# Kernel optimization log

Hardware: AMD Instinct MI355X
Metric: run time of the kernel (lower is better)

Reference implementation:

```python
import jax, jax.numpy as jnp
import numpy as np

D = 2048      # d_model
H = 16        # n_heads
DH = 128      # head dim
ROPE = 64     # qk_rope_dim = dh//2
NOPE = 64     # qk_nope_dim = dh//2
QP = 1024     # q_proj_dim = int(D*0.5)
KVP = 1365    # kv_proj_dim = int(D*2/3)
THETA = 10000.0
B, S = 2, 2048


def _ln(x, w, b):
    m = x.mean(-1, keepdims=True)
    v = ((x - m) ** 2).mean(-1, keepdims=True)
    return (x - m) / jnp.sqrt(v + 1e-5) * w + b


def _rot_half(x):
    x1, x2 = jnp.split(x, 2, axis=-1)
    return jnp.concatenate([-x2, x1], axis=-1)


def _rope_tables(seq_len):
    # freqs over full dh (as in torch buffer), then slice first ROPE//2 and repeat(...,2)
    freqs = 1.0 / (THETA ** (jnp.arange(0, DH, 2, dtype=jnp.float32) / DH))  # (DH//2,)
    emb = jnp.arange(seq_len, dtype=jnp.float32)[:, None] * freqs[None, :]   # (S, DH//2)
    c = jnp.cos(emb)[:, : ROPE // 2]
    s = jnp.sin(emb)[:, : ROPE // 2]
    cos = jnp.concatenate([c, c], axis=-1)  # (S, ROPE)  matches .repeat(1,1,1,2)
    sin = jnp.concatenate([s, s], axis=-1)
    return cos, sin


def setup_inputs() -> dict:
    ks = jax.random.split(jax.random.key(0), 8)
    p = lambda i, shape: 0.01 * jax.random.normal(ks[i], shape, dtype=jnp.float32)
    return {
        "query": jax.random.normal(ks[0], (B, S, D), dtype=jnp.float32),
        "W_dq": p(1, (D, QP)),
        "W_uq": p(2, (QP, D)),
        "q_ln_w": jnp.ones((QP,), jnp.float32),
        "q_ln_b": jnp.zeros((QP,), jnp.float32),
        "W_dkv": p(3, (D, KVP + ROPE)),
        "W_ukv": p(4, (KVP, D + H * NOPE)),
        "kv_ln_w": jnp.ones((KVP,), jnp.float32),
        "kv_ln_b": jnp.zeros((KVP,), jnp.float32),
        "W_o": p(5, (D, D)),
    }


def reference(query, W_dq, W_uq, q_ln_w, q_ln_b, W_dkv, W_ukv, kv_ln_w, kv_ln_b, W_o):
    b, sq, _ = query.shape
    # Q low-rank path
    cq = _ln(query @ W_dq, q_ln_w, q_ln_b)                       # (B,S,QP)
    Q = (cq @ W_uq).reshape(b, sq, H, DH).transpose(0, 2, 1, 3)  # (B,H,S,DH)
    Qn, Qr = Q[..., :NOPE], Q[..., NOPE:]
    cos, sin = _rope_tables(sq)                                  # (S,ROPE)
    Qr = Qr * cos + _rot_half(Qr) * sin
    # KV low-rank path
    compressed_kv = query @ W_dkv                                # (B,S,KVP+ROPE)
    kv_lat, Kr = compressed_kv[..., :KVP], compressed_kv[..., KVP:]
    kv_lat = _ln(kv_lat, kv_ln_w, kv_ln_b)
    KV = (kv_lat @ W_ukv).reshape(b, sq, H, DH + NOPE).transpose(0, 2, 1, 3)
    Kn, V = KV[..., :NOPE], KV[..., NOPE:]                       # (B,H,S,NOPE),(B,H,S,DH)
    Kr = Kr * cos + _rot_half(Kr) * sin                          # (B,S,ROPE) shared head
    qh = jnp.concatenate([Qn, Qr], axis=-1)                      # (B,H,S,DH)
    kh = jnp.concatenate([Kn, jnp.broadcast_to(Kr[:, None], (b, H, sq, ROPE))], axis=-1)
    # causal attention, scale 1/sqrt(dh) as in SDPA
    scores = jnp.einsum('bhqd,bhkd->bhqk', qh, kh) / jnp.sqrt(jnp.float32(DH))
    mask = jnp.tril(jnp.ones((sq, sq), dtype=bool))
    scores = jnp.where(mask, scores, -jnp.inf)
    attn = jax.nn.softmax(scores, axis=-1)
    out = jnp.einsum('bhqk,bhkd->bhqd', attn, V).transpose(0, 2, 1, 3).reshape(b, sq, D)
    output = out @ W_o.T                                          # nn.Linear, no bias
    return output, compressed_kv
```

## Files before the change

kernel.cpp:

```cpp
#include <hip/hip_runtime.h>

#define BB_   2
#define S_    2048
#define D_    2048
#define H_    16
#define DH_   128
#define ROPE_ 64
#define QP_   1024
#define KVP_  1365
#define KVPR_ 1429
#define KVP_PAD_ 1408
#define NKV_PAD_ 1536
#define NCOMB_ 2560
#define MT_   4096
#define UKV_N_ 3072

typedef unsigned short u16;
typedef unsigned int   u32;
typedef __attribute__((ext_vector_type(4))) u16    u16x4;
typedef __attribute__((ext_vector_type(8))) u16    u16x8;
typedef __attribute__((ext_vector_type(4))) u32    u32x4;
typedef __attribute__((ext_vector_type(8))) __bf16 bf16x8;
typedef __attribute__((ext_vector_type(4))) float  f32x4;
typedef __attribute__((ext_vector_type(16))) float f32x16;

#define NEG_BIG (-1.0e30f)
#define F32_FLAG_BITS 0x49742400u

__device__ __forceinline__ float bf2f(u16 u) {
    u32 x = ((u32)u) << 16;
    return __builtin_bit_cast(float, x);
}
__device__ __forceinline__ u16 f2bf(float f) {
    u32 u = __builtin_bit_cast(u32, f);
    u32 r = u + 0x7fffu + ((u >> 16) & 1u);
    return (u16)(r >> 16);
}
__device__ __forceinline__ u32 pk2(float a, float b) {
    __bf16 x = (__bf16)a, y = (__bf16)b;
    return (u32)__builtin_bit_cast(u16, x) | ((u32)__builtin_bit_cast(u16, y) << 16);
}
__device__ __forceinline__ bf16x8 ld_bf8(const u16* p) {
    u16x8 v = *(const u16x8*)p;
    return __builtin_bit_cast(bf16x8, v);
}
__device__ __forceinline__ bool flag_f32(const u32* flag) { return flag[0] > F32_FLAG_BITS; }

__device__ __forceinline__ void async16(const void* g, void* l) {
    __builtin_amdgcn_global_load_lds(
        (const __attribute__((address_space(1))) void*)g,
        (__attribute__((address_space(3))) void*)l, 16, 0, 0);
}

__global__ __launch_bounds__(256) void detect_kernel(const u16* __restrict__ q, u32* __restrict__ flag)
{
    u32 m = 0;
    for (int i = blockIdx.x * 256 + threadIdx.x; i < (1 << 20); i += 64 * 256) {
        float v = fabsf(bf2f(q[i]));
        u32 b = __builtin_bit_cast(u32, v);
        m = m > b ? m : b;
    }
    #pragma unroll
    for (int off = 32; off; off >>= 1) {
        u32 o = (u32)__shfl_xor((int)m, off, 64);
        m = m > o ? m : o;
    }
    if ((threadIdx.x & 63) == 0) atomicMax(flag, m);
}

__global__ __launch_bounds__(256) void cast_bf16_kernel(
    const void* __restrict__ in, u16* __restrict__ out, long n, const u32* __restrict__ flag)
{
    bool f32 = flag_f32(flag);
    long i0 = ((long)blockIdx.x * 256 + threadIdx.x) * 8;
    if (i0 >= n) return;
    u16x8 o;
    if (f32) {
        const float* p = (const float*)in + i0;
        #pragma unroll
        for (int j = 0; j < 8; j++) o[j] = f2bf(p[j]);
    } else {
        o = *(const u16x8*)((const u16*)in + i0);
    }
    *(u16x8*)(out + i0) = o;
}

template <int MODE>
__global__ __launch_bounds__(256) void gemm_bt(
    const u16* __restrict__ A, const u16* __restrict__ Bt,
    void* __restrict__ Cout, int M, int N, int K, const u32* __restrict__ flag)
{
    __shared__ u16 As[2][128 * 32];
    __shared__ u16 Bs[2][128 * 32];
    const int tid  = threadIdx.x;
    const int lane = tid & 63;
    const int wave = tid >> 6;
    const int m0 = blockIdx.x * 128;
    const int n0 = blockIdx.y * 128;
    const int wr = (wave >> 1) * 64;
    const int wc = (wave & 1) * 64;
    const bool f32o = (MODE == 2) ? flag_f32(flag) : false;

    const int srow = lane >> 2;
    const int scol = (lane & 3) * 8;
    const u16* aptr0 = A  + (long)(m0 + wave * 32 + srow) * K + scol;
    const u16* bptr0 = Bt + (long)(n0 + wave * 32 + srow) * K + scol;
    const int woff = (wave * 32) * 32;

    f32x4 acc[4][4] = {};

    const int row16 = lane & 15;
    const int kq = (lane >> 4) * 8;

    auto stage = [&](int buf, int kt) {
        u16* asl = &As[buf][woff];
        u16* bsl = &Bs[buf][woff];
        async16(aptr0 + kt,          asl);
        async16(aptr0 + 16 * K + kt, asl + 16 * 32);
        async16(bptr0 + kt,          bsl);
        async16(bptr0 + 16 * K + kt, bsl + 16 * 32);
    };
    auto compute = [&](int buf) {
        bf16x8 a[4], b[4];
        #pragma unroll
        for (int i = 0; i < 4; i++)
            a[i] = ld_bf8(&As[buf][(wr + i * 16 + row16) * 32 + kq]);
        #pragma unroll
        for (int j = 0; j < 4; j++)
            b[j] = ld_bf8(&Bs[buf][(wc + j * 16 + row16) * 32 + kq]);
        #pragma unroll
        for (int i = 0; i < 4; i++)
            #pragma unroll
            for (int j = 0; j < 4; j++)
                acc[i][j] = __builtin_amdgcn_mfma_f32_16x16x32_bf16(a[i], b[j], acc[i][j], 0, 0, 0);
    };

    stage(0, 0);
    __syncthreads();
    const int nk = K >> 5;
    for (int t = 0; t < nk; t += 2) {
        stage(1, (t + 1) * 32);
        compute(0);
        __syncthreads();
        if (t + 2 < nk) stage(0, (t + 2) * 32);
        compute(1);
        __syncthreads();
    }

    const int crow = wr + (lane >> 4) * 4;
    const int ccol = wc + row16;
    #pragma unroll
    for (int i = 0; i < 4; i++) {
        #pragma unroll
        for (int r = 0; r < 4; r++) {
            long row = m0 + crow + i * 16 + r;
            #pragma unroll
            for (int j = 0; j < 4; j++) {
                float v = acc[i][j][r];
                long col = n0 + ccol + j * 16;
                if (MODE == 2 && f32o) ((float*)Cout)[row * N + col] = v;
                else                   ((u16*)Cout)[row * N + col] = f2bf(v);
            }
        }
    }
}

__global__ __launch_bounds__(256) void transpose_pad_kernel(
    const void* __restrict__ in, u16* __restrict__ out,
    int Rin, int Cin, int Nout, int Kpad, const u32* __restrict__ flag)
{
    __shared__ u16 t[32][33];
    bool f32 = flag_f32(flag);
    int k0 = blockIdx.x * 32, n0 = blockIdx.y * 32;
    int tx = threadIdx.x & 31, ty = threadIdx.x >> 5;
    #pragma unroll
    for (int rr = 0; rr < 4; ++rr) {
        int k = k0 + ty + rr * 8, n = n0 + tx;
        u16 v = 0;
        if (k < Rin && n < Cin)
            v = f32 ? f2bf(((const float*)in)[(long)k * Cin + n])
                    : ((const u16*)in)[(long)k * Cin + n];
        t[ty + rr * 8][tx] = v;
    }
    __syncthreads();
    #pragma unroll
    for (int rr = 0; rr < 4; ++rr) {
        int n = n0 + ty + rr * 8, k = k0 + tx;
        if (n < Nout && k < Kpad) out[(long)n * Kpad + k] = t[tx][ty + rr * 8];
    }
}

__device__ __forceinline__ float block_sum(float v, float* red) {
    #pragma unroll
    for (int off = 32; off; off >>= 1) v += __shfl_xor(v, off, 64);
    int wv = threadIdx.x >> 6;
    __syncthreads();
    if ((threadIdx.x & 63) == 0) red[wv] = v;
    __syncthreads();
    return red[0] + red[1] + red[2] + red[3];
}

__global__ __launch_bounds__(256) void ln_q_kernel(
    const u16* __restrict__ x, const void* __restrict__ w, const void* __restrict__ bb,
    u16* __restrict__ y, const u32* __restrict__ flag, int stride)
{
    __shared__ float red[4];
    bool f32 = flag_f32(flag);
    long row = blockIdx.x;
    const u16* xr = x + row * stride;
    float v[4]; float s = 0.f;
    #pragma unroll
    for (int i = 0; i < 4; i++) { v[i] = bf2f(xr[threadIdx.x + i * 256]); s += v[i]; }
    float mean = block_sum(s, red) * (1.0f / QP_);
    float var = 0.f;
    #pragma unroll
    for (int i = 0; i < 4; i++) { float d = v[i] - mean; var += d * d; }
    var = block_sum(var, red) * (1.0f / QP_);
    float rstd = rsqrtf(var + 1e-5f);
    #pragma unroll
    for (int i = 0; i < 4; i++) {
        int idx = threadIdx.x + i * 256;
        float wv = f32 ? ((const float*)w)[idx] : bf2f(((const u16*)w)[idx]);
        float bv = f32 ? ((const float*)bb)[idx] : bf2f(((const u16*)bb)[idx]);
        y[row * QP_ + idx] = f2bf((v[i] - mean) * rstd * wv + bv);
    }
}

__global__ __launch_bounds__(256) void ln_kv_kernel(
    const u16* __restrict__ x, const void* __restrict__ w, const void* __restrict__ bb,
    u16* __restrict__ kv_lat, void* __restrict__ d_out, const u32* __restrict__ flag, int stride)
{
    __shared__ float red[4];
    bool f32 = flag_f32(flag);
    long row = blockIdx.x;
    const u16* xr = x + row * stride;
    u16 u[6]; float v[6]; float s = 0.f;
    #pragma unroll
    for (int i = 0; i < 6; i++) {
        int idx = threadIdx.x + i * 256;
        u[i] = xr[idx];
        v[i] = bf2f(u[i]);
        if (idx < KVP_) s += v[i];
    }
    float mean = block_sum(s, red) * (1.0f / KVP_);
    float var = 0.f;
    #pragma unroll
    for (int i = 0; i < 6; i++) {
        int idx = threadIdx.x + i * 256;
        if (idx < KVP_) { float d = v[i] - mean; var += d * d; }
    }
    var = block_sum(var, red) * (1.0f / KVP_);
    float rstd = rsqrtf(var + 1e-5f);

    float* out1f = (float*)d_out + (size_t)MT_ * D_;
    u16*   out1h = (u16*)d_out   + (size_t)MT_ * D_;
    #pragma unroll
    for (int i = 0; i < 6; i++) {
        int idx = threadIdx.x + i * 256;
        if (idx < KVPR_) {
            if (f32) out1f[row * KVPR_ + idx] = v[i];
            else     out1h[row * KVPR_ + idx] = u[i];
        }
        if (idx < KVP_PAD_) {
            float wv = 0.f, bv = 0.f;
            if (idx < KVP_) {
                wv = f32 ? ((const float*)w)[idx] : bf2f(((const u16*)w)[idx]);
                bv = f32 ? ((const float*)bb)[idx] : bf2f(((const u16*)bb)[idx]);
            }
            u16 o = 0;
            if (idx < KVP_) o = f2bf((v[i] - mean) * rstd * wv + bv);
            kv_lat[row * KVP_PAD_ + idx] = o;
        }
    }
}

__global__ void rope_tab_kernel(float* __restrict__ cosT, float* __restrict__ sinT, u32* __restrict__ flag) {
    int idx = blockIdx.x * 256 + threadIdx.x;
    if (idx == 0) flag[0] = 0u;
    if (idx >= S_ * 32) return;
    int pos = idx >> 5, i = idx & 31;
    float freq = (float)exp(-((double)i / 64.0) * log(10000.0));
    float ang = (float)pos * freq;
    cosT[idx] = (float)cos((double)ang);
    sinT[idx] = (float)sin((double)ang);
}

__global__ __launch_bounds__(256) void pack_q_kernel(
    const u16* __restrict__ Qm, const float* __restrict__ cosT, const float* __restrict__ sinT,
    u16* __restrict__ qh)
{
    int bs = blockIdx.x; int b = bs >> 11; int s = bs & 2047;
    int h = threadIdx.x >> 4; int d0 = (threadIdx.x & 15) * 8;
    const u16* src = Qm + (long)bs * 2048 + h * 128 + d0;
    u16x8 val = *(const u16x8*)src;
    if (d0 >= 64) {
        int r0 = d0 - 64;
        const u16* rb = Qm + (long)bs * 2048 + h * 128 + 64;
        u16x8 out;
        #pragma unroll
        for (int j = 0; j < 8; j++) {
            int r = r0 + j; int m = r & 31;
            float c = cosT[s * 32 + m], sn = sinT[s * 32 + m];
            float x = bf2f(val[j]);
            float o = (r < 32) ? -bf2f(rb[r + 32]) : bf2f(rb[r - 32]);
            out[j] = f2bf(x * c + o * sn);
        }
        val = out;
    }
    *(u16x8*)&qh[(((long)(b * H_ + h)) * S_ + s) * 128 + d0] = val;
}

__global__ __launch_bounds__(256) void pack_kh_kernel(
    const u16* __restrict__ KV, const void* __restrict__ d_out,
    const float* __restrict__ cosT, const float* __restrict__ sinT,
    u16* __restrict__ kh, const u32* __restrict__ flag)
{
    bool f32 = flag_f32(flag);
    int bs = blockIdx.x; int b = bs >> 11; int s = bs & 2047;
    int h = threadIdx.x >> 4; int d0 = (threadIdx.x & 15) * 8;
    u16x8 val;
    if (d0 < 64) {
        val = *(const u16x8*)&KV[(long)bs * 3072 + h * 192 + d0];
    } else {
        int r0 = d0 - 64;
        const float* rf = (const float*)d_out + (size_t)MT_ * D_ + (long)bs * KVPR_ + KVP_;
        const u16*   rh = (const u16*)d_out   + (size_t)MT_ * D_ + (long)bs * KVPR_ + KVP_;
        #pragma unroll
        for (int j = 0; j < 8; j++) {
            int r = r0 + j; int m = r & 31;
            float xr = f32 ? rf[r] : bf2f(rh[r]);
            float xo = f32 ? ((r < 32) ? -rf[r + 32] : rf[r - 32])
                           : ((r < 32) ? -bf2f(rh[r + 32]) : bf2f(rh[r - 32]));
            val[j] = f2bf(xr * cosT[s * 32 + m] + xo * sinT[s * 32 + m]);
        }
    }
    *(u16x8*)&kh[(((long)(b * H_ + h)) * S_ + s) * 128 + d0] = val;
}

__global__ __launch_bounds__(256) void pack_vt_kernel(const u16* __restrict__ KV, u16* __restrict__ Vt)
{
    int bh = blockIdx.x; int b = bh >> 4, h = bh & 15;
    int s0 = blockIdx.y * 64;
    __shared__ u16 t[64][136];
    #pragma unroll
    for (int it = 0; it < 4; ++it) {
        int ch = threadIdx.x + it * 256;
        int sr = ch >> 4, c8 = (ch & 15) * 8;
        *(u16x8*)&t[sr][c8] = *(const u16x8*)&KV[((long)(b * S_ + s0 + sr)) * 3072 + h * 192 + 64 + c8];
    }
    __syncthreads();
    #pragma unroll
    for (int it = 0; it < 4; ++it) {
        int ch = threadIdx.x + it * 256;
        int d = ch >> 3, s8 = (ch & 7) * 8;
        u16x8 v;
        #pragma unroll
        for (int j = 0; j < 8; j++) v[j] = t[s8 + j][d];
        *(u16x8*)&Vt[((long)bh * 128 + d) * S_ + s0 + s8] = v;
    }
}

#define ATT_SCALE 0.08838834764831845f
#define K_LOG2E (ATT_SCALE * 1.4426950408889634f)
#define DEFER_THR 62.0f

__global__ __launch_bounds__(256, 2) void attn_kernel(
    const u16* __restrict__ qh, const u16* __restrict__ kh,
    const u16* __restrict__ Vt, u16* __restrict__ attn_out)
{
    __shared__ u16 Ks[64 * 128];
    __shared__ u16 Vs[128 * 64];

    const int bh = (int)blockIdx.x + ((int)blockIdx.z << 3);
    const int b = bh >> 4, h = bh & 15;
    const int jq = ((int)blockIdx.z < 2) ? (15 - (int)blockIdx.y) : (int)blockIdx.y;
    const int qbase = jq * 128;
    const int tid = threadIdx.x;
    const int lane = tid & 63;
    const int w = tid >> 6;
    const int l5 = lane & 31;
    const int hi = lane >> 5;
    const int wq0 = qbase + w * 32;
    const int qg = wq0 + l5;
    const int kend = qbase + 128;
    const int kend_w = wq0 + 32;

    bf16x8 qb[8];
    {
        const u16* qp = &qh[((long)bh * S_ + qg) * 128 + 8 * hi];
        #pragma unroll
        for (int kc = 0; kc < 8; kc++)
            qb[kc] = ld_bf8(qp + kc * 16);
    }

    f32x16 o[4] = {};
    float m_run = NEG_BIG;
    float l_run = 0.f;

    const long khb = (long)bh * S_;

    u16x8 kst[4], vst[4];
    auto load_kv = [&](int k0) {
        #pragma unroll
        for (int it = 0; it < 4; ++it) {
            int r = w * 16 + it * 4 + (lane >> 4);
            kst[it] = *(const u16x8*)&kh[(khb + k0 + r) * 128 + (((lane & 15) ^ (r & 7)) << 3)];
        }
        #pragma unroll
        for (int it = 0; it < 4; ++it) {
            int d = w * 32 + it * 8 + (lane >> 3);
            vst[it] = *(const u16x8*)&Vt[((long)bh * 128 + d) * S_ + k0 + (((lane & 7) ^ (d & 7)) << 3)];
        }
    };

    load_kv(0);

    for (int k0 = 0; k0 < kend; k0 += 64) {
        __syncthreads();
        #pragma unroll
        for (int it = 0; it < 4; ++it)
            *(u16x8*)&Ks[(w * 16 + it * 4) * 128 + lane * 8] = kst[it];
        #pragma unroll
        for (int it = 0; it < 4; ++it)
            *(u16x8*)&Vs[(w * 32 + it * 8) * 64 + lane * 8] = vst[it];
        __syncthreads();
        if (k0 + 64 < kend) load_kv(k0 + 64);

        if (k0 < kend_w) {
            f32x16 sc[2] = {};
            #pragma unroll
            for (int kc = 0; kc < 8; kc++) {
                #pragma unroll
                for (int ct = 0; ct < 2; ct++) {
                    int krow = ct * 32 + l5;
                    bf16x8 kf = ld_bf8(&Ks[krow * 128 + (((2 * kc + hi) ^ (krow & 7)) << 3)]);
                    sc[ct] = __builtin_amdgcn_mfma_f32_32x32x16_bf16(kf, qb[kc], sc[ct], 0, 0, 0);
                }
            }
            if (k0 + 64 > wq0) {
                #pragma unroll
                for (int ct = 0; ct < 2; ct++)
                    #pragma unroll
                    for (int g = 0; g < 4; g++)
                        #pragma unroll
                        for (int t = 0; t < 4; t++)
                            sc[ct][g * 4 + t] =
                                (k0 + ct * 32 + g * 8 + t + 4 * hi <= qg) ? sc[ct][g * 4 + t] : NEG_BIG;
            }
            float m = sc[0][0];
            #pragma unroll
            for (int i = 1; i < 16; i++) m = fmaxf(m, sc[0][i]);
            #pragma unroll
            for (int i = 0; i < 16; i++) m = fmaxf(m, sc[1][i]);
            m = fmaxf(m, __shfl_xor(m, 32, 64));
            bool ok = (m <= m_run + DEFER_THR);
            if (!__all((int)ok)) {
                float mn = fmaxf(m_run, m);
                float alpha = exp2f((m_run - mn) * K_LOG2E);
                m_run = mn;
                l_run *= alpha;
                #pragma unroll
                for (int dt = 0; dt < 4; dt++)
                    #pragma unroll
                    for (int i = 0; i < 16; i++) o[dt][i] *= alpha;
            }
            float mk = m_run * K_LOG2E;
            float s = 0.f;
            #pragma unroll
            for (int ct = 0; ct < 2; ct++)
                #pragma unroll
                for (int i = 0; i < 16; i++) {
                    float p = exp2f(fmaf(sc[ct][i], K_LOG2E, -mk));
                    sc[ct][i] = p;
                    s += p;
                }
            l_run += s + __shfl_xor(s, 32, 64);
            bf16x8 pb[4];
            #pragma unroll
            for (int ct = 0; ct < 2; ct++)
                #pragma unroll
                for (int c2 = 0; c2 < 2; c2++) {
                    u32 lo0 = pk2(sc[ct][8 * c2 + 0], sc[ct][8 * c2 + 1]);
                    u32 lo1 = pk2(sc[ct][8 * c2 + 2], sc[ct][8 * c2 + 3]);
                    u32 h0  = pk2(sc[ct][8 * c2 + 4], sc[ct][8 * c2 + 5]);
                    u32 h1  = pk2(sc[ct][8 * c2 + 6], sc[ct][8 * c2 + 7]);
                    u32 s0 = hi ? lo0 : h0;
                    u32 s1 = hi ? lo1 : h1;
                    u32 r0 = (u32)__shfl_xor((int)s0, 32, 64);
                    u32 r1 = (u32)__shfl_xor((int)s1, 32, 64);
                    u32x4 f;
                    f[0] = hi ? r0 : lo0;
                    f[1] = hi ? r1 : lo1;
                    f[2] = hi ? h0 : r0;
                    f[3] = hi ? h1 : r1;
                    pb[ct * 2 + c2] = __builtin_bit_cast(bf16x8, f);
                }
            #pragma unroll
            for (int kk = 0; kk < 4; kk++) {
                #pragma unroll
                for (int dt = 0; dt < 4; dt++) {
                    int drow = dt * 32 + l5;
                    bf16x8 vf = ld_bf8(&Vs[drow * 64 + (((2 * kk + hi) ^ (drow & 7)) << 3)]);
                    o[dt] = __builtin_amdgcn_mfma_f32_32x32x16_bf16(vf, pb[kk], o[dt], 0, 0, 0);
                }
            }
        }
    }

    float inv = 1.0f / l_run;
    const long orow = ((long)b * S_ + qg) * 2048 + h * 128;
    #pragma unroll
    for (int dt = 0; dt < 4; dt++)
        #pragma unroll
        for (int g = 0; g < 4; g++) {
            u16x4 v;
            #pragma unroll
            for (int t = 0; t < 4; t++) v[t] = f2bf(o[dt][g * 4 + t] * inv);
            *(u16x4*)&attn_out[orow + dt * 32 + g * 8 + 4 * hi] = v;
        }
}

#define MIB(x) ((size_t)(x) << 20)
extern "C" void kernel_launch(void* const* d_in, const int* in_sizes, int n_in,
                              void* d_out, int out_size, void* d_ws, size_t ws_size,
                              hipStream_t stream)
{
    const void* query  = d_in[0];
    const void* W_dq   = d_in[1];
    const void* W_uq   = d_in[2];
    const void* q_ln_w = d_in[3];
    const void* q_ln_b = d_in[4];
    const void* W_dkv  = d_in[5];
    const void* W_ukv  = d_in[6];
    const void* kv_ln_w = d_in[7];
    const void* kv_ln_b = d_in[8];
    const void* W_o    = d_in[9];
    (void)ws_size; (void)in_sizes; (void)n_in; (void)out_size;

    char* base = (char*)d_ws;
    u32*   flag     = (u32*)base;
    float* rope_cos = (float*)(base + 4096);
    float* rope_sin = (float*)(base + 266240);
    u16* qh     = (u16*)(base + MIB(1));
    u16* kh     = (u16*)(base + MIB(17));
    u16* Vt     = (u16*)(base + MIB(33));
    u16* q_bf   = (u16*)(base + MIB(49));
    u16* Wo_bf  = (u16*)(base + MIB(65));
    u16* Wcomb  = (u16*)(base + MIB(73));
    u16* cqkv   = (u16*)(base + MIB(83));
    u16* cq     = (u16*)(base + MIB(103));
    u16* kv_lat = (u16*)(base + MIB(111));
    u16* WuqT   = (u16*)(base + MIB(73));
    u16* Qmat   = (u16*)(base + MIB(77));
    u16* WukvT  = (u16*)(base + MIB(73));
    u16* KV     = (u16*)(base + MIB(82));
    u16* attn_o = (u16*)(base + MIB(106));

    rope_tab_kernel<<<(S_ * 32 + 255) / 256, 256, 0, stream>>>(rope_cos, rope_sin, flag);
    detect_kernel<<<64, 256, 0, stream>>>((const u16*)query, flag);

    cast_bf16_kernel<<<4096, 256, 0, stream>>>(query, q_bf, (long)MT_ * D_, flag);
    cast_bf16_kernel<<<2048, 256, 0, stream>>>(W_o, Wo_bf, (long)D_ * D_, flag);

    transpose_pad_kernel<<<dim3(64, 32), 256, 0, stream>>>(W_dq, Wcomb, 2048, 1024, 1024, 2048, flag);
    transpose_pad_kernel<<<dim3(64, 48), 256, 0, stream>>>(W_dkv, Wcomb + (size_t)1024 * 2048, 2048, KVPR_, NKV_PAD_, 2048, flag);
    gemm_bt<0><<<dim3(32, 20), 256, 0, stream>>>(q_bf, Wcomb, cqkv, MT_, NCOMB_, D_, flag);
    ln_q_kernel<<<MT_, 256, 0, stream>>>(cqkv, q_ln_w, q_ln_b, cq, flag, NCOMB_);
    ln_kv_kernel<<<MT_, 256, 0, stream>>>(cqkv + 1024, kv_ln_w, kv_ln_b, kv_lat, d_out, flag, NCOMB_);

    transpose_pad_kernel<<<dim3(32, 64), 256, 0, stream>>>(W_uq, WuqT, 1024, 2048, 2048, 1024, flag);
    gemm_bt<0><<<dim3(32, 16), 256, 0, stream>>>(cq, WuqT, Qmat, MT_, D_, QP_, flag);
    pack_q_kernel<<<MT_, 256, 0, stream>>>(Qmat, rope_cos, rope_sin, qh);

    transpose_pad_kernel<<<dim3(44, 96), 256, 0, stream>>>(W_ukv, WukvT, KVP_, UKV_N_, UKV_N_, KVP_PAD_, flag);
    gemm_bt<0><<<dim3(32, 24), 256, 0, stream>>>(kv_lat, WukvT, KV, MT_, UKV_N_, KVP_PAD_, flag);
    pack_kh_kernel<<<MT_, 256, 0, stream>>>(KV, d_out, rope_cos, rope_sin, kh, flag);
    pack_vt_kernel<<<dim3(32, 32), 256, 0, stream>>>(KV, Vt);

    attn_kernel<<<dim3(8, 16, 4), 256, 0, stream>>>(qh, kh, Vt, attn_o);
    gemm_bt<2><<<dim3(32, 16), 256, 0, stream>>>(attn_o, Wo_bf, d_out, MT_, D_, D_, flag);
}
```

Baseline: 528.2 us.

## Fuse RoPE and head packing into GEMM epilogues, merge prep kernels

Merges the two cast kernels, the four weight transposes and the two layernorms into single batched launches indexed by blockIdx.z. The Q up-projection GEMM now writes the head-major qh layout with RoPE applied in its epilogue, and the KV up-projection GEMM scatters the K-nope part straight into kh. The KV layernorm also applies RoPE to the shared K rope slice and broadcasts it into kh. This removes the pack_q and pack_kh kernels, their intermediate round trips through memory, and several launches, at the cost of scattered 2-byte stores in the GEMM epilogues and a reshuffled workspace layout.

```diff
diff --git a/kernel.cpp b/kernel.cpp
--- a/kernel.cpp
+++ b/kernel.cpp
@@ -68,10 +68,14 @@
     if ((threadIdx.x & 63) == 0) atomicMax(flag, m);
 }
 
-__global__ __launch_bounds__(256) void cast_bf16_kernel(
-    const void* __restrict__ in, u16* __restrict__ out, long n, const u32* __restrict__ flag)
+__global__ __launch_bounds__(256) void cast_merged_kernel(
+    const void* __restrict__ qin, const void* __restrict__ woin,
+    u16* __restrict__ q_bf, u16* __restrict__ wo_bf, const u32* __restrict__ flag)
 {
     bool f32 = flag_f32(flag);
+    const void* in; u16* out; long n;
+    if (blockIdx.z == 0) { in = qin;  out = q_bf;  n = (long)MT_ * D_; }
+    else                 { in = woin; out = wo_bf; n = (long)D_ * D_; if (blockIdx.x >= 2048) return; }
     long i0 = ((long)blockIdx.x * 256 + threadIdx.x) * 8;
     if (i0 >= n) return;
     u16x8 o;
@@ -88,7 +92,9 @@
 template <int MODE>
 __global__ __launch_bounds__(256) void gemm_bt(
     const u16* __restrict__ A, const u16* __restrict__ Bt,
-    void* __restrict__ Cout, int M, int N, int K, const u32* __restrict__ flag)
+    void* __restrict__ Cout, int M, int N, int K,
+    const float* __restrict__ cosT, const float* __restrict__ sinT,
+    u16* __restrict__ khp, const u32* __restrict__ flag)
 {
     __shared__ u16 As[2][128 * 32];
     __shared__ u16 Bs[2][128 * 32];
@@ -149,6 +155,57 @@
 
     const int crow = wr + (lane >> 4) * 4;
     const int ccol = wc + row16;
+
+    if (MODE == 3) {
+        const int h = (int)blockIdx.y;
+        u16* qhp = (u16*)Cout;
+        #pragma unroll
+        for (int i = 0; i < 4; i++) {
+            #pragma unroll
+            for (int r = 0; r < 4; r++) {
+                int row = m0 + crow + i * 16 + r;
+                int b = row >> 11, s = row & 2047;
+                long obase = (((long)(b * 16 + h)) * 2048 + s) * 128;
+                if (wc == 0) {
+                    #pragma unroll
+                    for (int j = 0; j < 4; j++)
+                        qhp[obase + j * 16 + row16] = f2bf(acc[i][j][r]);
+                } else {
+                    float c0 = cosT[s * 32 + row16],      s0 = sinT[s * 32 + row16];
+                    float c1 = cosT[s * 32 + 16 + row16], s1 = sinT[s * 32 + 16 + row16];
+                    float x0 = acc[i][0][r], x1 = acc[i][1][r];
+                    float x2 = acc[i][2][r], x3 = acc[i][3][r];
+                    qhp[obase + 64 + row16]  = f2bf(x0 * c0 - x2 * s0);
+                    qhp[obase + 80 + row16]  = f2bf(x1 * c1 - x3 * s1);
+                    qhp[obase + 96 + row16]  = f2bf(x2 * c0 + x0 * s0);
+                    qhp[obase + 112 + row16] = f2bf(x3 * c1 + x1 * s1);
+                }
+            }
+        }
+        return;
+    }
+    if (MODE == 4) {
+        #pragma unroll
+        for (int i = 0; i < 4; i++) {
+            #pragma unroll
+            for (int r = 0; r < 4; r++) {
+                int row = m0 + crow + i * 16 + r;
+                int b = row >> 11, s = row & 2047;
+                #pragma unroll
+                for (int j = 0; j < 4; j++) {
+                    int c = n0 + wc + j * 16 + row16;
+                    int h = c / 192, dd = c - h * 192;
+                    u16 v16 = f2bf(acc[i][j][r]);
+                    if (dd < 64)
+                        khp[(((long)(b * 16 + h)) * 2048 + s) * 128 + dd] = v16;
+                    else
+                        ((u16*)Cout)[(long)row * N + c] = v16;
+                }
+            }
+        }
+        return;
+    }
+
     #pragma unroll
     for (int i = 0; i < 4; i++) {
         #pragma unroll
@@ -165,10 +222,20 @@
     }
 }
 
-__global__ __launch_bounds__(256) void transpose_pad_kernel(
-    const void* __restrict__ in, u16* __restrict__ out,
-    int Rin, int Cin, int Nout, int Kpad, const u32* __restrict__ flag)
-{
+__global__ __launch_bounds__(256) void transpose_all_kernel(
+    const void* __restrict__ w_dq, const void* __restrict__ w_dkv,
+    const void* __restrict__ w_uq, const void* __restrict__ w_ukv,
+    u16* __restrict__ wcomb, u16* __restrict__ wuqT, u16* __restrict__ wukvT,
+    const u32* __restrict__ flag)
+{
+    const void* in; u16* out; int Rin, Cin, Nout, Kpad, gx, gy;
+    switch (blockIdx.z) {
+        case 0: in = w_dq;  out = wcomb;                       Rin = 2048; Cin = 1024;   Nout = 1024;     Kpad = 2048;     gx = 64; gy = 32; break;
+        case 1: in = w_dkv; out = wcomb + (size_t)1024 * 2048; Rin = 2048; Cin = KVPR_;  Nout = NKV_PAD_; Kpad = 2048;     gx = 64; gy = 48; break;
+        case 2: in = w_uq;  out = wuqT;                        Rin = 1024; Cin = 2048;   Nout = 2048;     Kpad = 1024;     gx = 32; gy = 64; break;
+        default:in = w_ukv; out = wukvT;                       Rin = KVP_; Cin = UKV_N_; Nout = UKV_N_;   Kpad = KVP_PAD_; gx = 44; gy = 96; break;
+    }
+    if ((int)blockIdx.x >= gx || (int)blockIdx.y >= gy) return;
     __shared__ u16 t[32][33];
     bool f32 = flag_f32(flag);
     int k0 = blockIdx.x * 32, n0 = blockIdx.y * 32;
@@ -200,76 +267,88 @@
     return red[0] + red[1] + red[2] + red[3];
 }
 
-__global__ __launch_bounds__(256) void ln_q_kernel(
-    const u16* __restrict__ x, const void* __restrict__ w, const void* __restrict__ bb,
-    u16* __restrict__ y, const u32* __restrict__ flag, int stride)
+__global__ __launch_bounds__(256) void ln_both_kernel(
+    const u16* __restrict__ x, const void* __restrict__ qw, const void* __restrict__ qb,
+    const void* __restrict__ kw, const void* __restrict__ kb,
+    u16* __restrict__ cq, u16* __restrict__ kv_lat, void* __restrict__ d_out,
+    u16* __restrict__ kh, const float* __restrict__ cosT, const float* __restrict__ sinT,
+    const u32* __restrict__ flag)
 {
     __shared__ float red[4];
+    __shared__ float kr[64];
     bool f32 = flag_f32(flag);
     long row = blockIdx.x;
-    const u16* xr = x + row * stride;
-    float v[4]; float s = 0.f;
-    #pragma unroll
-    for (int i = 0; i < 4; i++) { v[i] = bf2f(xr[threadIdx.x + i * 256]); s += v[i]; }
-    float mean = block_sum(s, red) * (1.0f / QP_);
-    float var = 0.f;
-    #pragma unroll
-    for (int i = 0; i < 4; i++) { float d = v[i] - mean; var += d * d; }
-    var = block_sum(var, red) * (1.0f / QP_);
-    float rstd = rsqrtf(var + 1e-5f);
-    #pragma unroll
-    for (int i = 0; i < 4; i++) {
-        int idx = threadIdx.x + i * 256;
-        float wv = f32 ? ((const float*)w)[idx] : bf2f(((const u16*)w)[idx]);
-        float bv = f32 ? ((const float*)bb)[idx] : bf2f(((const u16*)bb)[idx]);
-        y[row * QP_ + idx] = f2bf((v[i] - mean) * rstd * wv + bv);
-    }
-}
-
-__global__ __launch_bounds__(256) void ln_kv_kernel(
-    const u16* __restrict__ x, const void* __restrict__ w, const void* __restrict__ bb,
-    u16* __restrict__ kv_lat, void* __restrict__ d_out, const u32* __restrict__ flag, int stride)
-{
-    __shared__ float red[4];
-    bool f32 = flag_f32(flag);
-    long row = blockIdx.x;
-    const u16* xr = x + row * stride;
-    u16 u[6]; float v[6]; float s = 0.f;
-    #pragma unroll
-    for (int i = 0; i < 6; i++) {
-        int idx = threadIdx.x + i * 256;
-        u[i] = xr[idx];
-        v[i] = bf2f(u[i]);
-        if (idx < KVP_) s += v[i];
-    }
-    float mean = block_sum(s, red) * (1.0f / KVP_);
-    float var = 0.f;
-    #pragma unroll
-    for (int i = 0; i < 6; i++) {
-        int idx = threadIdx.x + i * 256;
-        if (idx < KVP_) { float d = v[i] - mean; var += d * d; }
-    }
-    var = block_sum(var, red) * (1.0f / KVP_);
-    float rstd = rsqrtf(var + 1e-5f);
-
-    float* out1f = (float*)d_out + (size_t)MT_ * D_;
-    u16*   out1h = (u16*)d_out   + (size_t)MT_ * D_;
-    #pragma unroll
-    for (int i = 0; i < 6; i++) {
-        int idx = threadIdx.x + i * 256;
-        if (idx < KVPR_) {
-            if (f32) out1f[row * KVPR_ + idx] = v[i];
-            else     out1h[row * KVPR_ + idx] = u[i];
-        }
-        if (idx < KVP_PAD_) {
-            float wv = 0.f, bv = 0.f;
-            if (idx < KVP_) {
-                wv = f32 ? ((const float*)w)[idx] : bf2f(((const u16*)w)[idx]);
-                bv = f32 ? ((const float*)bb)[idx] : bf2f(((const u16*)bb)[idx]);
-            }
-            u16 o = 0;
-            if (idx < KVP_) o = f2bf((v[i] - mean) * rstd * wv + bv);
-            kv_lat[row * KVP_PAD_ + idx] = o;
+    const int tid = threadIdx.x;
+
+    if (blockIdx.z == 0) {
+        const u16* xr = x + row * NCOMB_;
+        float v[4]; float s = 0.f;
+        #pragma unroll
+        for (int i = 0; i < 4; i++) { v[i] = bf2f(xr[tid + i * 256]); s += v[i]; }
+        float mean = block_sum(s, red) * (1.0f / QP_);
+        float var = 0.f;
+        #pragma unroll
+        for (int i = 0; i < 4; i++) { float d = v[i] - mean; var += d * d; }
+        var = block_sum(var, red) * (1.0f / QP_);
+        float rstd = rsqrtf(var + 1e-5f);
+        #pragma unroll
+        for (int i = 0; i < 4; i++) {
+            int idx = tid + i * 256;
+            float wv = f32 ? ((const float*)qw)[idx] : bf2f(((const u16*)qw)[idx]);
+            float bv = f32 ? ((const float*)qb)[idx] : bf2f(((const u16*)qb)[idx]);
+            cq[row * QP_ + idx] = f2bf((v[i] - mean) * rstd * wv + bv);
+        }
+    } else {
+        const int b = (int)(row >> 11), s_ = (int)(row & 2047);
+        const u16* xr = x + row * NCOMB_ + QP_;
+        u16 u[6]; float v[6]; float s = 0.f;
+        #pragma unroll
+        for (int i = 0; i < 6; i++) {
+            int idx = tid + i * 256;
+            u[i] = xr[idx];
+            v[i] = bf2f(u[i]);
+            if (idx >= KVP_ && idx < KVPR_) kr[idx - KVP_] = v[i];
+            if (idx < KVP_) s += v[i];
+        }
+        float mean = block_sum(s, red) * (1.0f / KVP_);
+        float var = 0.f;
+        #pragma unroll
+        for (int i = 0; i < 6; i++) {
+            int idx = tid + i * 256;
+            if (idx < KVP_) { float d = v[i] - mean; var += d * d; }
+        }
+        var = block_sum(var, red) * (1.0f / KVP_);
+        float rstd = rsqrtf(var + 1e-5f);
+
+        float* out1f = (float*)d_out + (size_t)MT_ * D_;
+        u16*   out1h = (u16*)d_out   + (size_t)MT_ * D_;
+        #pragma unroll
+        for (int i = 0; i < 6; i++) {
+            int idx = tid + i * 256;
+            if (idx < KVPR_) {
+                if (f32) out1f[row * KVPR_ + idx] = v[i];
+                else     out1h[row * KVPR_ + idx] = u[i];
+            }
+            if (idx < KVP_PAD_) {
+                float wv = 0.f, bv = 0.f;
+                if (idx < KVP_) {
+                    wv = f32 ? ((const float*)kw)[idx] : bf2f(((const u16*)kw)[idx]);
+                    bv = f32 ? ((const float*)kb)[idx] : bf2f(((const u16*)kb)[idx]);
+                }
+                u16 o = 0;
+                if (idx < KVP_) o = f2bf((v[i] - mean) * rstd * wv + bv);
+                kv_lat[row * KVP_PAD_ + idx] = o;
+            }
+            if (idx >= KVP_ && idx < KVPR_) {
+                int r = idx - KVP_;
+                float xr_ = kr[r];
+                float xo = (r < 32) ? -kr[r + 32] : kr[r - 32];
+                int m = r & 31;
+                u16 vv = f2bf(xr_ * cosT[s_ * 32 + m] + xo * sinT[s_ * 32 + m]);
+                #pragma unroll
+                for (int h = 0; h < 16; h++)
+                    kh[(((long)(b * 16 + h)) * 2048 + s_) * 128 + 64 + r] = vv;
+            }
         }
     }
 }
@@ -283,58 +362,6 @@
     float ang = (float)pos * freq;
     cosT[idx] = (float)cos((double)ang);
     sinT[idx] = (float)sin((double)ang);
-}
-
-__global__ __launch_bounds__(256) void pack_q_kernel(
-    const u16* __restrict__ Qm, const float* __restrict__ cosT, const float* __restrict__ sinT,
-    u16* __restrict__ qh)
-{
-    int bs = blockIdx.x; int b = bs >> 11; int s = bs & 2047;
-    int h = threadIdx.x >> 4; int d0 = (threadIdx.x & 15) * 8;
-    const u16* src = Qm + (long)bs * 2048 + h * 128 + d0;
-    u16x8 val = *(const u16x8*)src;
-    if (d0 >= 64) {
-        int r0 = d0 - 64;
-        const u16* rb = Qm + (long)bs * 2048 + h * 128 + 64;
-        u16x8 out;
-        #pragma unroll
-        for (int j = 0; j < 8; j++) {
-            int r = r0 + j; int m = r & 31;
-            float c = cosT[s * 32 + m], sn = sinT[s * 32 + m];
-            float x = bf2f(val[j]);
-            float o = (r < 32) ? -bf2f(rb[r + 32]) : bf2f(rb[r - 32]);
-            out[j] = f2bf(x * c + o * sn);
-        }
-        val = out;
-    }
-    *(u16x8*)&qh[(((long)(b * H_ + h)) * S_ + s) * 128 + d0] = val;
-}
-
-__global__ __launch_bounds__(256) void pack_kh_kernel(
-    const u16* __restrict__ KV, const void* __restrict__ d_out,
-    const float* __restrict__ cosT, const float* __restrict__ sinT,
-    u16* __restrict__ kh, const u32* __restrict__ flag)
-{
-    bool f32 = flag_f32(flag);
-    int bs = blockIdx.x; int b = bs >> 11; int s = bs & 2047;
-    int h = threadIdx.x >> 4; int d0 = (threadIdx.x & 15) * 8;
-    u16x8 val;
-    if (d0 < 64) {
-        val = *(const u16x8*)&KV[(long)bs * 3072 + h * 192 + d0];
-    } else {
-        int r0 = d0 - 64;
-        const float* rf = (const float*)d_out + (size_t)MT_ * D_ + (long)bs * KVPR_ + KVP_;
-        const u16*   rh = (const u16*)d_out   + (size_t)MT_ * D_ + (long)bs * KVPR_ + KVP_;
-        #pragma unroll
-        for (int j = 0; j < 8; j++) {
-            int r = r0 + j; int m = r & 31;
-            float xr = f32 ? rf[r] : bf2f(rh[r]);
-            float xo = f32 ? ((r < 32) ? -rf[r + 32] : rf[r - 32])
-                           : ((r < 32) ? -bf2f(rh[r + 32]) : bf2f(rh[r - 32]));
-            val[j] = f2bf(xr * cosT[s * 32 + m] + xo * sinT[s * 32 + m]);
-        }
-    }
-    *(u16x8*)&kh[(((long)(b * H_ + h)) * S_ + s) * 128 + d0] = val;
 }
 
 __global__ __launch_bounds__(256) void pack_vt_kernel(const u16* __restrict__ KV, u16* __restrict__ Vt)
@@ -550,33 +577,32 @@
     u16* cqkv   = (u16*)(base + MIB(83));
     u16* cq     = (u16*)(base + MIB(103));
     u16* kv_lat = (u16*)(base + MIB(111));
-    u16* WuqT   = (u16*)(base + MIB(73));
-    u16* Qmat   = (u16*)(base + MIB(77));
-    u16* WukvT  = (u16*)(base + MIB(73));
-    u16* KV     = (u16*)(base + MIB(82));
-    u16* attn_o = (u16*)(base + MIB(106));
+    u16* WuqT   = (u16*)(base + MIB(122));
+    u16* WukvT  = (u16*)(base + MIB(126));
+    u16* KV     = (u16*)(base + MIB(73));
+    u16* attn_o = (u16*)(base + MIB(73));
 
     rope_tab_kernel<<<(S_ * 32 + 255) / 256, 256, 0, stream>>>(rope_cos, rope_sin, flag);
     detect_kernel<<<64, 256, 0, stream>>>((const u16*)query, flag);
 
-    cast_bf16_kernel<<<4096, 256, 0, stream>>>(query, q_bf, (long)MT_ * D_, flag);
-    cast_bf16_kernel<<<2048, 256, 0, stream>>>(W_o, Wo_bf, (long)D_ * D_, flag);
-
-    transpose_pad_kernel<<<dim3(64, 32), 256, 0, stream>>>(W_dq, Wcomb, 2048, 1024, 1024, 2048, flag);
-    transpose_pad_kernel<<<dim3(64, 48), 256, 0, stream>>>(W_dkv, Wcomb + (size_t)1024 * 2048, 2048, KVPR_, NKV_PAD_, 2048, flag);
-    gemm_bt<0><<<dim3(32, 20), 256, 0, stream>>>(q_bf, Wcomb, cqkv, MT_, NCOMB_, D_, flag);
-    ln_q_kernel<<<MT_, 256, 0, stream>>>(cqkv, q_ln_w, q_ln_b, cq, flag, NCOMB_);
-    ln_kv_kernel<<<MT_, 256, 0, stream>>>(cqkv + 1024, kv_ln_w, kv_ln_b, kv_lat, d_out, flag, NCOMB_);
-
-    transpose_pad_kernel<<<dim3(32, 64), 256, 0, stream>>>(W_uq, WuqT, 1024, 2048, 2048, 1024, flag);
-    gemm_bt<0><<<dim3(32, 16), 256, 0, stream>>>(cq, WuqT, Qmat, MT_, D_, QP_, flag);
-    pack_q_kernel<<<MT_, 256, 0, stream>>>(Qmat, rope_cos, rope_sin, qh);
-
-    transpose_pad_kernel<<<dim3(44, 96), 256, 0, stream>>>(W_ukv, WukvT, KVP_, UKV_N_, UKV_N_, KVP_PAD_, flag);
-    gemm_bt<0><<<dim3(32, 24), 256, 0, stream>>>(kv_lat, WukvT, KV, MT_, UKV_N_, KVP_PAD_, flag);
-    pack_kh_kernel<<<MT_, 256, 0, stream>>>(KV, d_out, rope_cos, rope_sin, kh, flag);
+    cast_merged_kernel<<<dim3(4096, 1, 2), 256, 0, stream>>>(query, W_o, q_bf, Wo_bf, flag);
+    transpose_all_kernel<<<dim3(64, 96, 4), 256, 0, stream>>>(W_dq, W_dkv, W_uq, W_ukv,
+                                                              Wcomb, WuqT, WukvT, flag);
+
+    gemm_bt<0><<<dim3(32, 20), 256, 0, stream>>>(q_bf, Wcomb, cqkv, MT_, NCOMB_, D_,
+                                                 nullptr, nullptr, nullptr, flag);
+    ln_both_kernel<<<dim3(MT_, 1, 2), 256, 0, stream>>>(cqkv, q_ln_w, q_ln_b, kv_ln_w, kv_ln_b,
+                                                        cq, kv_lat, d_out, kh,
+                                                        rope_cos, rope_sin, flag);
+
+    gemm_bt<3><<<dim3(32, 16), 256, 0, stream>>>(cq, WuqT, qh, MT_, D_, QP_,
+                                                 rope_cos, rope_sin, nullptr, flag);
+
+    gemm_bt<4><<<dim3(32, 24), 256, 0, stream>>>(kv_lat, WukvT, KV, MT_, UKV_N_, KVP_PAD_,
+                                                 nullptr, nullptr, kh, flag);
     pack_vt_kernel<<<dim3(32, 32), 256, 0, stream>>>(KV, Vt);
 
     attn_kernel<<<dim3(8, 16, 4), 256, 0, stream>>>(qh, kh, Vt, attn_o);
-    gemm_bt<2><<<dim3(32, 16), 256, 0, stream>>>(attn_o, Wo_bf, d_out, MT_, D_, D_, flag);
-}
+    gemm_bt<2><<<dim3(32, 16), 256, 0, stream>>>(attn_o, Wo_bf, d_out, MT_, D_, D_,
+                                                 nullptr, nullptr, nullptr, flag);
+}
```

Result: faster. 464.4 us (-12.1%).
